# Performance work log

Measured on AMD Instinct MI355X. Metric: run time of the kernel, lower is better.

The kernel has to match this reference:

```python
import jax, jax.numpy as jnp
import numpy as np

H = 100  # hidden size of both LSTM layers (fixed in the module)

def lstm_layer(x, w_ih, w_hh, b_ih, b_hh):
    # x: [B, T, I]; w_ih: [4H, I]; w_hh: [4H, H]; biases: [4H]
    # PyTorch gate order: input, forget, cell(g), output.
    B, T, _ = x.shape
    xg = jnp.einsum('bti,gi->btg', x, w_ih) + b_ih + b_hh  # [B, T, 4H], input GEMM hoisted out of the scan
    h0 = jnp.zeros((B, H), x.dtype)
    c0 = jnp.zeros((B, H), x.dtype)
    w_hh_t = w_hh.T  # [H, 4H]

    def step(carry, xg_t):
        h, c = carry
        g = xg_t + h @ w_hh_t                # [B, 4H]
        i, f, gg, o = jnp.split(g, 4, axis=-1)
        i = jax.nn.sigmoid(i)
        f = jax.nn.sigmoid(f)
        gg = jnp.tanh(gg)
        o = jax.nn.sigmoid(o)
        c = f * c + i * gg
        h = o * jnp.tanh(c)
        return (h, c), h

    _, hs = jax.lax.scan(step, (h0, c0), jnp.swapaxes(xg, 0, 1))  # hs: [T, B, H]
    return jnp.swapaxes(hs, 0, 1)  # [B, T, H]


def setup_inputs() -> dict:
    key = jax.random.key(0)
    ks = jax.random.split(key, 13)
    B, T, I = 256, 2048, 8
    s = lambda fan: 1.0 / np.sqrt(fan)
    u = lambda k, shape, fan: jax.random.uniform(k, shape, jnp.float32, -s(fan), s(fan))
    return {
        'x': jax.random.normal(ks[0], (B, T, I), jnp.float32),
        'w_ih1': u(ks[1], (4 * H, I), H), 'w_hh1': u(ks[2], (4 * H, H), H),
        'b_ih1': u(ks[3], (4 * H,), H), 'b_hh1': u(ks[4], (4 * H,), H),
        'w_ih2': u(ks[5], (4 * H, H), H), 'w_hh2': u(ks[6], (4 * H, H), H),
        'b_ih2': u(ks[7], (4 * H,), H), 'b_hh2': u(ks[8], (4 * H,), H),
        'fc1_w': u(ks[9], (25, H), H), 'fc1_b': u(ks[10], (25,), H),
        'fc2_w': u(ks[11], (1, 25), 25), 'fc2_b': u(ks[12], (1,), 25),
    }


def reference(x, w_ih1, w_hh1, b_ih1, b_hh1, w_ih2, w_hh2, b_ih2, b_hh2,
              fc1_w, fc1_b, fc2_w, fc2_b):
    # Dropout layers are identity in eval mode.
    h1 = lstm_layer(x, w_ih1, w_hh1, b_ih1, b_hh1)    # [B, T, H]
    h2 = lstm_layer(h1, w_ih2, w_hh2, b_ih2, b_hh2)   # [B, T, H]
    last = h2[:, -1, :]                               # [B, H]
    y = last @ fc1_w.T + fc1_b                        # [B, 25]
    return y @ fc2_w.T + fc2_b                        # [B, 1]
```

## Files before the change

### kernel.cpp

```cpp
#include <hip/hip_runtime.h>

#define BB 256
#define TT 2048
#define HD 100

typedef _Float16 h2v __attribute__((ext_vector_type(2)));

__device__ __forceinline__ float fdot2(unsigned w, unsigned h, float c) {
#if __has_builtin(__builtin_amdgcn_fdot2)
    return __builtin_amdgcn_fdot2(__builtin_bit_cast(h2v, w),
                                  __builtin_bit_cast(h2v, h), c, false);
#else
    h2v a = __builtin_bit_cast(h2v, w), b = __builtin_bit_cast(h2v, h);
    c = fmaf((float)a[0], (float)b[0], c);
    c = fmaf((float)a[1], (float)b[1], c);
    return c;
#endif
}
__device__ __forceinline__ unsigned packh2(float a, float b) {
    h2v p; p[0] = (_Float16)a; p[1] = (_Float16)b;
    return __builtin_bit_cast(unsigned, p);
}
__device__ __forceinline__ float rcp_f(float x) {
#if __has_builtin(__builtin_amdgcn_rcpf)
    return __builtin_amdgcn_rcpf(x);
#else
    return 1.0f / x;
#endif
}
__device__ __forceinline__ float act_f(float x, float m, float s, float d) {
    return fmaf(m, rcp_f(1.0f + __expf(-s * x)), d);
}
__device__ __forceinline__ float tanh_f(float x) {
    return fmaf(2.0f, rcp_f(1.0f + __expf(-2.0f * x)), -1.0f);
}

__global__ __launch_bounds__(512)
__attribute__((amdgpu_waves_per_eu(2, 2)))
void lstm_fused(
    const float* __restrict__ x,
    const float* __restrict__ w_ih1, const float* __restrict__ w_hh1,
    const float* __restrict__ b_ih1, const float* __restrict__ b_hh1,
    const float* __restrict__ w_ih2, const float* __restrict__ w_hh2,
    const float* __restrict__ b_ih2, const float* __restrict__ b_hh2,
    const float* __restrict__ fc1_w, const float* __restrict__ fc1_b,
    const float* __restrict__ fc2_w, const float* __restrict__ fc2_b,
    float* __restrict__ out)
{
    const int b    = blockIdx.x;
    const int tid  = threadIdx.x;
    const int lane = tid & 63;
    const int grp  = tid >> 8;
    const int lt   = tid & 255;

    __shared__ unsigned h1p[64];
    __shared__ unsigned h2p[64];
    __shared__ __align__(16) unsigned xs[2][32][4];
    __shared__ float g1[400];
    __shared__ float g2[400];
    __shared__ float h2f[HD];
    __shared__ float fca[25];

    const bool isG = lt < 200;
    const int  gt  = isG ? lt : 199;
    const int  um  = lt >> 2;
    const bool isU = ((lt & 3) == 3) && isG;
    const bool isX = (grp == 0) && (lt >= 200) && (lt < 232);
    const int  xsl = lt - 200;

    unsigned wreg[200];
    float bias0, bias1, cc0 = 0.f, cc1 = 0.f;

    const int g0 = 2 * gt, g1r = 2 * gt + 1;
    if (grp == 0) {
        { const float4* p = (const float4*)(w_ih1 + (size_t)g0 * 8);
          float4 v0 = p[0], v1 = p[1];
          wreg[0] = packh2(v0.x, v0.y); wreg[1] = packh2(v0.z, v0.w);
          wreg[2] = packh2(v1.x, v1.y); wreg[3] = packh2(v1.z, v1.w); }
        { const float4* p = (const float4*)(w_ih1 + (size_t)g1r * 8);
          float4 v0 = p[0], v1 = p[1];
          wreg[54] = packh2(v0.x, v0.y); wreg[55] = packh2(v0.z, v0.w);
          wreg[56] = packh2(v1.x, v1.y); wreg[57] = packh2(v1.z, v1.w); }
        { const float4* p = (const float4*)(w_hh1 + (size_t)g0 * HD);
          #pragma unroll
          for (int q = 0; q < 25; ++q) {
              float4 v = p[q];
              wreg[4 + 2*q] = packh2(v.x, v.y); wreg[5 + 2*q] = packh2(v.z, v.w);
          } }
        { const float4* p = (const float4*)(w_hh1 + (size_t)g1r * HD);
          #pragma unroll
          for (int q = 0; q < 25; ++q) {
              float4 v = p[q];
              wreg[58 + 2*q] = packh2(v.x, v.y); wreg[59 + 2*q] = packh2(v.z, v.w);
          } }
        bias0 = b_ih1[g0] + b_hh1[g0];
        bias1 = b_ih1[g1r] + b_hh1[g1r];
    } else {
        { const float4* p = (const float4*)(w_ih2 + (size_t)g0 * HD);
          #pragma unroll
          for (int q = 0; q < 25; ++q) {
              float4 v = p[q];
              wreg[2*q] = packh2(v.x, v.y); wreg[2*q + 1] = packh2(v.z, v.w);
          } }
        { const float4* p = (const float4*)(w_ih2 + (size_t)g1r * HD);
          #pragma unroll
          for (int q = 0; q < 25; ++q) {
              float4 v = p[q];
              wreg[50 + 2*q] = packh2(v.x, v.y); wreg[51 + 2*q] = packh2(v.z, v.w);
          } }
        { const float4* p = (const float4*)(w_hh2 + (size_t)g0 * HD);
          #pragma unroll
          for (int q = 0; q < 25; ++q) {
              float4 v = p[q];
              wreg[100 + 2*q] = packh2(v.x, v.y); wreg[101 + 2*q] = packh2(v.z, v.w);
          } }
        { const float4* p = (const float4*)(w_hh2 + (size_t)g1r * HD);
          #pragma unroll
          for (int q = 0; q < 25; ++q) {
              float4 v = p[q];
              wreg[150 + 2*q] = packh2(v.x, v.y); wreg[151 + 2*q] = packh2(v.z, v.w);
          } }
        bias0 = b_ih2[g0] + b_hh2[g0];
        bias1 = b_ih2[g1r] + b_hh2[g1r];
    }
    const bool tg = (gt >= 100) && (gt < 150);
    const float am = tg ? 2.0f : 1.0f;
    const float as = tg ? 2.0f : 1.0f;
    const float ad = tg ? -1.0f : 0.0f;

    if (tid < 64) { h1p[tid] = 0u; h2p[tid] = 0u; }
    if (isX) {
        const float4* p = (const float4*)(x + ((size_t)b * TT + xsl) * 8);
        float4 v0 = p[0], v1 = p[1];
        xs[0][xsl][0] = packh2(v0.x, v0.y); xs[0][xsl][1] = packh2(v0.z, v0.w);
        xs[0][xsl][2] = packh2(v1.x, v1.y); xs[0][xsl][3] = packh2(v1.z, v1.w);
    }
    __syncthreads();

    float4 pa = {0,0,0,0}, pb = {0,0,0,0};

    #pragma unroll 1
    for (int i = 0; i <= TT; ++i) {
        const bool pf = ((i & 31) == 0) && (i + 32 < TT);
        if (grp == 0) {
            if (i < TT) {
                if (isX && pf) {
                    const float4* p = (const float4*)(x + ((size_t)b * TT + i + 32 + xsl) * 8);
                    pa = p[0]; pb = p[1];
                }
                const unsigned st = h1p[lane];
                const unsigned* xq = xs[(i >> 5) & 1][i & 31];
                unsigned x0 = xq[0], x1 = xq[1], x2 = xq[2], x3 = xq[3];
                float a0 = bias0, a1 = bias1, a2 = 0.f, a3 = 0.f;
                a0 = fdot2(wreg[0], x0, a0); a2 = fdot2(wreg[1], x1, a2);
                a0 = fdot2(wreg[2], x2, a0); a2 = fdot2(wreg[3], x3, a2);
                a1 = fdot2(wreg[54], x0, a1); a3 = fdot2(wreg[55], x1, a3);
                a1 = fdot2(wreg[56], x2, a1); a3 = fdot2(wreg[57], x3, a3);
                #pragma unroll
                for (int k = 0; k < 50; ++k) {
                    unsigned hk = (unsigned)__builtin_amdgcn_readlane((int)st, k);
                    if (k & 1) { a2 = fdot2(wreg[4 + k], hk, a2); a3 = fdot2(wreg[58 + k], hk, a3); }
                    else       { a0 = fdot2(wreg[4 + k], hk, a0); a1 = fdot2(wreg[58 + k], hk, a1); }
                }
                float r0 = act_f(a0 + a2, am, as, ad);
                float r1 = act_f(a1 + a3, am, as, ad);
                if (isG) *(float2*)(g1 + 2 * gt) = make_float2(r0, r1);
            }
        } else {
            if (i >= 1) {
                const unsigned cur = h1p[lane];
                const unsigned st2 = h2p[lane];
                float a0 = bias0, a1 = bias1, a2 = 0.f, a3 = 0.f;
                #pragma unroll
                for (int k = 0; k < 50; ++k) {
                    unsigned hk = (unsigned)__builtin_amdgcn_readlane((int)cur, k);
                    if (k & 1) { a2 = fdot2(wreg[k], hk, a2); a3 = fdot2(wreg[50 + k], hk, a3); }
                    else       { a0 = fdot2(wreg[k], hk, a0); a1 = fdot2(wreg[50 + k], hk, a1); }
                }
                #pragma unroll
                for (int k = 0; k < 50; ++k) {
                    unsigned hk = (unsigned)__builtin_amdgcn_readlane((int)st2, k);
                    if (k & 1) { a2 = fdot2(wreg[100 + k], hk, a2); a3 = fdot2(wreg[150 + k], hk, a3); }
                    else       { a0 = fdot2(wreg[100 + k], hk, a0); a1 = fdot2(wreg[150 + k], hk, a1); }
                }
                float r0 = act_f(a0 + a2, am, as, ad);
                float r1 = act_f(a1 + a3, am, as, ad);
                if (isG) *(float2*)(g2 + 2 * gt) = make_float2(r0, r1);
            }
        }
        __syncthreads();
        if (grp == 0) {
            if (i < TT) {
                if (isU) {
                    const int j = 2 * um;
                    float2 gi = *(const float2*)(g1 + j);
                    float2 gf = *(const float2*)(g1 + 100 + j);
                    float2 gg = *(const float2*)(g1 + 200 + j);
                    float2 go = *(const float2*)(g1 + 300 + j);
                    cc0 = gf.x * cc0 + gi.x * gg.x;
                    cc1 = gf.y * cc1 + gi.y * gg.y;
                    float h0 = go.x * tanh_f(cc0);
                    float h1v = go.y * tanh_f(cc1);
                    h1p[um] = packh2(h0, h1v);
                }
                if (isX && pf) {
                    const int nb2 = ((i >> 5) + 1) & 1;
                    xs[nb2][xsl][0] = packh2(pa.x, pa.y); xs[nb2][xsl][1] = packh2(pa.z, pa.w);
                    xs[nb2][xsl][2] = packh2(pb.x, pb.y); xs[nb2][xsl][3] = packh2(pb.z, pb.w);
                }
            }
        } else {
            if (i >= 1 && isU) {
                const int j = 2 * um;
                float2 gi = *(const float2*)(g2 + j);
                float2 gf = *(const float2*)(g2 + 100 + j);
                float2 gg = *(const float2*)(g2 + 200 + j);
                float2 go = *(const float2*)(g2 + 300 + j);
                cc0 = gf.x * cc0 + gi.x * gg.x;
                cc1 = gf.y * cc1 + gi.y * gg.y;
                float h0 = go.x * tanh_f(cc0);
                float h1v = go.y * tanh_f(cc1);
                h2p[um] = packh2(h0, h1v);
                if (i == TT) { h2f[j] = h0; h2f[j + 1] = h1v; }
            }
        }
        __syncthreads();
    }

    if (tid < 25) {
        float a = fc1_b[tid];
        const float* wp = fc1_w + tid * HD;
        #pragma unroll
        for (int k = 0; k < HD; ++k) a += h2f[k] * wp[k];
        fca[tid] = a;
    }
    __syncthreads();
    if (tid == 0) {
        float y = fc2_b[0];
        #pragma unroll
        for (int m = 0; m < 25; ++m) y += fca[m] * fc2_w[m];
        out[b] = y;
    }
}

extern "C" void kernel_launch(void* const* d_in, const int* in_sizes, int n_in,
                              void* d_out, int out_size, void* d_ws, size_t ws_size,
                              hipStream_t stream) {
    const float* x     = (const float*)d_in[0];
    const float* w_ih1 = (const float*)d_in[1];
    const float* w_hh1 = (const float*)d_in[2];
    const float* b_ih1 = (const float*)d_in[3];
    const float* b_hh1 = (const float*)d_in[4];
    const float* w_ih2 = (const float*)d_in[5];
    const float* w_hh2 = (const float*)d_in[6];
    const float* b_ih2 = (const float*)d_in[7];
    const float* b_hh2 = (const float*)d_in[8];
    const float* fc1_w = (const float*)d_in[9];
    const float* fc1_b = (const float*)d_in[10];
    const float* fc2_w = (const float*)d_in[11];
    const float* fc2_b = (const float*)d_in[12];
    float* out = (float*)d_out;

    lstm_fused<<<BB, 512, 0, stream>>>(x, w_ih1, w_hh1, b_ih1, b_hh1,
                                       w_ih2, w_hh2, b_ih2, b_hh2,
                                       fc1_w, fc1_b, fc2_w, fc2_b, out);
}
```

Measured before the change: 2.751 ms.

## Keep LSTM hidden state in registers and drop second per-step barrier

Every wave now recomputes the cell and hidden update redundantly for its own lanes and keeps the packed hidden state in a register, instead of one thread per four publishing it through shared memory. The gate buffers are double-buffered, so only one __syncthreads per timestep is needed rather than two. This removes a barrier and a shared-memory round trip from the serial recurrence. In exchange, every wave does extra redundant activation math and holds more state in registers.

```diff
diff --git a/kernel.cpp b/kernel.cpp
--- a/kernel.cpp
+++ b/kernel.cpp
@@ -36,7 +36,7 @@
 }
 
 __global__ __launch_bounds__(512)
-__attribute__((amdgpu_waves_per_eu(2, 2)))
+__attribute__((amdgpu_flat_work_group_size(512, 512), amdgpu_waves_per_eu(2, 2)))
 void lstm_fused(
     const float* __restrict__ x,
     const float* __restrict__ w_ih1, const float* __restrict__ w_hh1,
@@ -53,23 +53,22 @@
     const int grp  = tid >> 8;
     const int lt   = tid & 255;
 
-    __shared__ unsigned h1p[64];
-    __shared__ unsigned h2p[64];
     __shared__ __align__(16) unsigned xs[2][32][4];
-    __shared__ float g1[400];
-    __shared__ float g2[400];
+    __shared__ float g1b[2][400];
+    __shared__ float g2b[2][400];
     __shared__ float h2f[HD];
     __shared__ float fca[25];
 
     const bool isG = lt < 200;
     const int  gt  = isG ? lt : 199;
-    const int  um  = lt >> 2;
-    const bool isU = ((lt & 3) == 3) && isG;
     const bool isX = (grp == 0) && (lt >= 200) && (lt < 232);
     const int  xsl = lt - 200;
 
     unsigned wreg[200];
-    float bias0, bias1, cc0 = 0.f, cc1 = 0.f;
+    float bias0, bias1;
+    float c1x = 0.f, c1y = 0.f;
+    float c2x = 0.f, c2y = 0.f;
+    unsigned h1reg = 0u, h2reg = 0u;
 
     const int g0 = 2 * gt, g1r = 2 * gt + 1;
     if (grp == 0) {
@@ -128,7 +127,6 @@
     const float as = tg ? 2.0f : 1.0f;
     const float ad = tg ? -1.0f : 0.0f;
 
-    if (tid < 64) { h1p[tid] = 0u; h2p[tid] = 0u; }
     if (isX) {
         const float4* p = (const float4*)(x + ((size_t)b * TT + xsl) * 8);
         float4 v0 = p[0], v1 = p[1];
@@ -142,13 +140,14 @@
     #pragma unroll 1
     for (int i = 0; i <= TT; ++i) {
         const bool pf = ((i & 31) == 0) && (i + 32 < TT);
+        const int  bf = i & 1;
         if (grp == 0) {
             if (i < TT) {
                 if (isX && pf) {
                     const float4* p = (const float4*)(x + ((size_t)b * TT + i + 32 + xsl) * 8);
                     pa = p[0]; pb = p[1];
                 }
-                const unsigned st = h1p[lane];
+                const unsigned st = h1reg;
                 const unsigned* xq = xs[(i >> 5) & 1][i & 31];
                 unsigned x0 = xq[0], x1 = xq[1], x2 = xq[2], x3 = xq[3];
                 float a0 = bias0, a1 = bias1, a2 = 0.f, a3 = 0.f;
@@ -164,12 +163,12 @@
                 }
                 float r0 = act_f(a0 + a2, am, as, ad);
                 float r1 = act_f(a1 + a3, am, as, ad);
-                if (isG) *(float2*)(g1 + 2 * gt) = make_float2(r0, r1);
+                if (isG) *(float2*)(&g1b[bf][2 * gt]) = make_float2(r0, r1);
             }
         } else {
             if (i >= 1) {
-                const unsigned cur = h1p[lane];
-                const unsigned st2 = h2p[lane];
+                const unsigned cur = h1reg;
+                const unsigned st2 = h2reg;
                 float a0 = bias0, a1 = bias1, a2 = 0.f, a3 = 0.f;
                 #pragma unroll
                 for (int k = 0; k < 50; ++k) {
@@ -185,47 +184,42 @@
                 }
                 float r0 = act_f(a0 + a2, am, as, ad);
                 float r1 = act_f(a1 + a3, am, as, ad);
-                if (isG) *(float2*)(g2 + 2 * gt) = make_float2(r0, r1);
+                if (isG) *(float2*)(&g2b[bf][2 * gt]) = make_float2(r0, r1);
             }
         }
         __syncthreads();
-        if (grp == 0) {
-            if (i < TT) {
-                if (isU) {
-                    const int j = 2 * um;
-                    float2 gi = *(const float2*)(g1 + j);
-                    float2 gf = *(const float2*)(g1 + 100 + j);
-                    float2 gg = *(const float2*)(g1 + 200 + j);
-                    float2 go = *(const float2*)(g1 + 300 + j);
-                    cc0 = gf.x * cc0 + gi.x * gg.x;
-                    cc1 = gf.y * cc1 + gi.y * gg.y;
-                    float h0 = go.x * tanh_f(cc0);
-                    float h1v = go.y * tanh_f(cc1);
-                    h1p[um] = packh2(h0, h1v);
-                }
-                if (isX && pf) {
-                    const int nb2 = ((i >> 5) + 1) & 1;
-                    xs[nb2][xsl][0] = packh2(pa.x, pa.y); xs[nb2][xsl][1] = packh2(pa.z, pa.w);
-                    xs[nb2][xsl][2] = packh2(pb.x, pb.y); xs[nb2][xsl][3] = packh2(pb.z, pb.w);
-                }
+        if (i < TT && lane < 50) {
+            const float* g = g1b[bf];
+            float2 gi = *(const float2*)(g + 2 * lane);
+            float2 gf = *(const float2*)(g + 100 + 2 * lane);
+            float2 gg = *(const float2*)(g + 200 + 2 * lane);
+            float2 go = *(const float2*)(g + 300 + 2 * lane);
+            c1x = gf.x * c1x + gi.x * gg.x;
+            c1y = gf.y * c1y + gi.y * gg.y;
+            h1reg = packh2(go.x * tanh_f(c1x), go.y * tanh_f(c1y));
+        }
+        if (grp == 1 && i >= 1 && lane < 50) {
+            const float* g = g2b[bf];
+            float2 gi = *(const float2*)(g + 2 * lane);
+            float2 gf = *(const float2*)(g + 100 + 2 * lane);
+            float2 gg = *(const float2*)(g + 200 + 2 * lane);
+            float2 go = *(const float2*)(g + 300 + 2 * lane);
+            c2x = gf.x * c2x + gi.x * gg.x;
+            c2y = gf.y * c2y + gi.y * gg.y;
+            float h0 = go.x * tanh_f(c2x);
+            float h1v = go.y * tanh_f(c2y);
+            h2reg = packh2(h0, h1v);
+            if (i == TT) {
+                h2f[2 * lane] = h0; h2f[2 * lane + 1] = h1v;
             }
-        } else {
-            if (i >= 1 && isU) {
-                const int j = 2 * um;
-                float2 gi = *(const float2*)(g2 + j);
-                float2 gf = *(const float2*)(g2 + 100 + j);
-                float2 gg = *(const float2*)(g2 + 200 + j);
-                float2 go = *(const float2*)(g2 + 300 + j);
-                cc0 = gf.x * cc0 + gi.x * gg.x;
-                cc1 = gf.y * cc1 + gi.y * gg.y;
-                float h0 = go.x * tanh_f(cc0);
-                float h1v = go.y * tanh_f(cc1);
-                h2p[um] = packh2(h0, h1v);
-                if (i == TT) { h2f[j] = h0; h2f[j + 1] = h1v; }
-            }
-        }
-        __syncthreads();
-    }
+        }
+        if (isX && pf) {
+            const int nb2 = ((i >> 5) + 1) & 1;
+            xs[nb2][xsl][0] = packh2(pa.x, pa.y); xs[nb2][xsl][1] = packh2(pa.z, pa.w);
+            xs[nb2][xsl][2] = packh2(pb.x, pb.y); xs[nb2][xsl][3] = packh2(pb.z, pb.w);
+        }
+    }
+    __syncthreads();
 
     if (tid < 25) {
         float a = fc1_b[tid];
```

Result: no change. 2.790 ms (+1.4%).
